# Kernel optimization log

Hardware: AMD Instinct MI355X
Metric: run time of the kernel (lower is better)

Reference implementation:

```python
import jax, jax.numpy as jnp
import numpy as np

TOP_K = 8  # num_experts_per_tok


def setup_inputs() -> dict:
    key = jax.random.key(0)
    k1, k2 = jax.random.split(key)
    hidden_states = jax.random.normal(k1, (4, 4096, 2048), dtype=jnp.float32)
    weight = jax.random.normal(k2, (128, 2048), dtype=jnp.float32) * 0.02
    return {"hidden_states": hidden_states, "weight": weight}


def reference(hidden_states, weight):
    B, S, H = hidden_states.shape
    x = hidden_states.reshape(-1, H).astype(jnp.float32)        # [T, H], T = B*S
    logits = jnp.einsum("th,eh->te", x, weight.astype(jnp.float32))  # [T, E]
    scores = jax.nn.softmax(logits, axis=-1)                    # float32 softmax
    topk_weight, topk_idx = jax.lax.top_k(scores, TOP_K)        # [T, K]
    # norm_topk_prob=True: renormalize selected probabilities
    topk_weight = topk_weight / jnp.sum(topk_weight, axis=-1, keepdims=True)
    return topk_idx, topk_weight
```

## Files before the change

### kernel.cpp

```cpp
#include <hip/hip_runtime.h>
#include <math.h>

#define T_TOKENS 16384
#define HDIM     2048
#define NEXP     128
#define TOPK     8

#define BK    64
#define NCH   (HDIM / BK)
#define KPAD  72

#define F16_MIN_NORM    6.1035156e-05f
#define SPLIT_SCALE     4096.0f
#define INV_SPLIT_SCALE 2.44140625e-04f

typedef __attribute__((ext_vector_type(8))) _Float16 f16x8;
typedef __attribute__((ext_vector_type(4))) float    f32x4;

__device__ __forceinline__ void f16split(float f, _Float16& hi, _Float16& lo) {
    _Float16 h = (_Float16)f;
    float back = (float)h;
    if (fabsf(f) < F16_MIN_NORM) { h = (_Float16)0.f; back = 0.f; }
    lo = (_Float16)((f - back) * SPLIT_SCALE);
    hi = h;
}

__global__ __launch_bounds__(256) void pack_w(const float* __restrict__ w,
                                              unsigned short* __restrict__ wp1,
                                              unsigned short* __restrict__ wp2) {
    int p = blockIdx.x * 256 + threadIdx.x;
    int lane = p & 63, nt = (p >> 6) & 7, kk = p >> 9;
    int col = lane & 15, quad = lane >> 4;
    const float* src = w + (size_t)(nt * 16 + col) * HDIM + kk * 32 + quad * 8;
    unsigned short h[8], l[8];
#pragma unroll
    for (int j = 0; j < 8; ++j) {
        _Float16 hh, ll;
        f16split(src[j], hh, ll);
        union { _Float16 x; unsigned short u; } ch, cl;
        ch.x = hh; cl.x = ll;
        h[j] = ch.u; l[j] = cl.u;
    }
    *(uint4*)(wp1 + (size_t)p * 8) = *(const uint4*)h;
    *(uint4*)(wp2 + (size_t)p * 8) = *(const uint4*)l;
}

__global__ __launch_bounds__(256, 2) void moe_gate(const float* __restrict__ x,
                                                   const unsigned short* __restrict__ wp1,
                                                   const unsigned short* __restrict__ wp2,
                                                   float* __restrict__ out_idx,
                                                   float* __restrict__ out_w) {
    __shared__ __align__(16) unsigned char smem[18432];
    unsigned short* xbuf[2][2];
    xbuf[0][0] = (unsigned short*)smem;
    xbuf[0][1] = (unsigned short*)(smem + 4608);
    xbuf[1][0] = (unsigned short*)(smem + 9216);
    xbuf[1][1] = (unsigned short*)(smem + 13824);
    float* epil = (float*)smem;

    const int tid  = threadIdx.x;
    const int lane = tid & 63;
    const int wv   = tid >> 6;
    const int col  = lane & 15;
    const int quad = lane >> 4;
    const long tok0 = (long)blockIdx.x * 32;

    const int srow = tid >> 3, scol = (tid & 7) * 8;
    const float* xg = x + (tok0 + srow) * HDIM + scol;
    const int swoff = srow * KPAD + scol;

    f32x4 acc[2][2], accc[2][2];
#pragma unroll
    for (int m = 0; m < 2; ++m)
#pragma unroll
        for (int n = 0; n < 2; ++n) { acc[m][n] = (f32x4){0,0,0,0}; accc[m][n] = (f32x4){0,0,0,0}; }

    float4 xv0, xv1;

    auto cvt_store = [&](int buf) {
        const float f[8] = {xv0.x, xv0.y, xv0.z, xv0.w, xv1.x, xv1.y, xv1.z, xv1.w};
        unsigned short h[8], l[8];
#pragma unroll
        for (int j = 0; j < 8; ++j) {
            _Float16 hh, ll;
            f16split(f[j], hh, ll);
            union { _Float16 x; unsigned short u; } ch, cl;
            ch.x = hh; cl.x = ll;
            h[j] = ch.u; l[j] = cl.u;
        }
        *(uint4*)(xbuf[buf][0] + swoff) = *(const uint4*)h;
        *(uint4*)(xbuf[buf][1] + swoff) = *(const uint4*)l;
    };

    xv0 = *(const float4*)(xg);
    xv1 = *(const float4*)(xg + 4);
    cvt_store(0);
    __syncthreads();

    for (int ch = 0; ch < NCH; ++ch) {
        const int cur = ch & 1;
        if (ch + 1 < NCH) {
            xv0 = *(const float4*)(xg + (ch + 1) * BK);
            xv1 = *(const float4*)(xg + (ch + 1) * BK + 4);
        }

        f16x8 b1[2][2], b2[2][2];
#pragma unroll
        for (int ks = 0; ks < 2; ++ks)
#pragma unroll
            for (int n = 0; n < 2; ++n) {
                const size_t off = ((size_t)((2 * ch + ks) * 8 + (wv * 2 + n)) * 64 + lane) * 8;
                b1[ks][n] = *(const f16x8*)(wp1 + off);
                b2[ks][n] = *(const f16x8*)(wp2 + off);
            }

#pragma unroll
        for (int ks = 0; ks < 2; ++ks) {
            f16x8 a1[2], a2[2];
#pragma unroll
            for (int m = 0; m < 2; ++m) {
                const int ao = (m * 16 + col) * KPAD + ks * 32 + quad * 8;
                a1[m] = *(const f16x8*)(xbuf[cur][0] + ao);
                a2[m] = *(const f16x8*)(xbuf[cur][1] + ao);
            }
#pragma unroll
            for (int m = 0; m < 2; ++m)
#pragma unroll
                for (int n = 0; n < 2; ++n) {
                    acc[m][n]  = __builtin_amdgcn_mfma_f32_16x16x32_f16(a1[m], b1[ks][n], acc[m][n],  0, 0, 0);
                    accc[m][n] = __builtin_amdgcn_mfma_f32_16x16x32_f16(a1[m], b2[ks][n], accc[m][n], 0, 0, 0);
                    accc[m][n] = __builtin_amdgcn_mfma_f32_16x16x32_f16(a2[m], b1[ks][n], accc[m][n], 0, 0, 0);
                }
        }

        if (ch + 1 < NCH) cvt_store(cur ^ 1);
        __syncthreads();
    }

#pragma unroll
    for (int m = 0; m < 2; ++m)
#pragma unroll
        for (int n = 0; n < 2; ++n)
#pragma unroll
            for (int r = 0; r < 4; ++r)
                epil[(m * 16 + quad * 4 + r) * 132 + wv * 32 + n * 16 + col] =
                    acc[m][n][r] + accc[m][n][r] * INV_SPLIT_SCALE;
    __syncthreads();

    for (int i = 0; i < 8; ++i) {
        const int t = wv * 8 + i;
        float2 p = *(const float2*)(epil + t * 132 + 2 * lane);
        float v0 = p.x, v1 = p.y;
        const int i0 = 2 * lane, i1 = 2 * lane + 1;

        float topv[TOPK];
        int topi[TOPK];
#pragma unroll
        for (int s = 0; s < TOPK; ++s) {
            float mv = (v0 >= v1) ? v0 : v1;
            int   mi = (v0 >= v1) ? i0 : i1;
#pragma unroll
            for (int off = 32; off >= 1; off >>= 1) {
                float ov = __shfl_xor(mv, off);
                int   oi = __shfl_xor(mi, off);
                if (ov > mv || (ov == mv && oi < mi)) { mv = ov; mi = oi; }
            }
            topv[s] = mv; topi[s] = mi;
            if (i0 == mi) v0 = -INFINITY;
            if (i1 == mi) v1 = -INFINITY;
        }

        const float m = topv[0];
        float sum = 0.f;
#pragma unroll
        for (int s = 0; s < TOPK; ++s) sum += expf(topv[s] - m);
        const float inv = 1.f / sum;

        float myv = topv[0]; int myi = topi[0];
#pragma unroll
        for (int s = 1; s < TOPK; ++s)
            if (lane == s) { myv = topv[s]; myi = topi[s]; }

        if (lane < TOPK) {
            long tok = tok0 + t;
            out_idx[tok * TOPK + lane] = (float)myi;
            out_w[tok * TOPK + lane]   = expf(myv - m) * inv;
        }
    }
}

extern "C" void kernel_launch(void* const* d_in, const int* in_sizes, int n_in,
                              void* d_out, int out_size, void* d_ws, size_t ws_size,
                              hipStream_t stream) {
    const float* x = (const float*)d_in[0];
    const float* w = (const float*)d_in[1];
    float* out = (float*)d_out;

    unsigned short* wp1 = (unsigned short*)d_ws;
    unsigned short* wp2 = wp1 + (size_t)NEXP * HDIM;

    pack_w<<<(64 * 8 * 64) / 256, 256, 0, stream>>>(w, wp1, wp2);
    moe_gate<<<T_TOKENS / 32, 256, 0, stream>>>(x, wp1, wp2, out, out + (size_t)T_TOKENS * TOPK);
}
```

Before: 264.8 us.

## Split K across waves per 16-token block and reduce partials in shared memory

```diff
diff --git a/kernel.cpp b/kernel.cpp
--- a/kernel.cpp
+++ b/kernel.cpp
@@ -6,9 +6,11 @@
 #define NEXP     128
 #define TOPK     8
 
-#define BK    64
-#define NCH   (HDIM / BK)
-#define KPAD  72
+#define KSPLIT   4
+#define KRANGE   (HDIM / KSPLIT)
+#define BK       64
+#define NCHW     (KRANGE / BK)
+#define KPAD     72
 
 #define F16_MIN_NORM    6.1035156e-05f
 #define SPLIT_SCALE     4096.0f
@@ -16,6 +18,7 @@
 
 typedef __attribute__((ext_vector_type(8))) _Float16 f16x8;
 typedef __attribute__((ext_vector_type(4))) float    f32x4;
+typedef __attribute__((ext_vector_type(4))) float    f32x4v;
 
 __device__ __forceinline__ void f16split(float f, _Float16& hi, _Float16& lo) {
     _Float16 h = (_Float16)f;
@@ -45,17 +48,12 @@
     *(uint4*)(wp2 + (size_t)p * 8) = *(const uint4*)l;
 }
 
-__global__ __launch_bounds__(256, 2) void moe_gate(const float* __restrict__ x,
+__global__ __launch_bounds__(256, 4) void moe_gate(const float* __restrict__ x,
                                                    const unsigned short* __restrict__ wp1,
                                                    const unsigned short* __restrict__ wp2,
                                                    float* __restrict__ out_idx,
                                                    float* __restrict__ out_w) {
-    __shared__ __align__(16) unsigned char smem[18432];
-    unsigned short* xbuf[2][2];
-    xbuf[0][0] = (unsigned short*)smem;
-    xbuf[0][1] = (unsigned short*)(smem + 4608);
-    xbuf[1][0] = (unsigned short*)(smem + 9216);
-    xbuf[1][1] = (unsigned short*)(smem + 13824);
+    __shared__ __align__(16) unsigned char smem[33792];
     float* epil = (float*)smem;
 
     const int tid  = threadIdx.x;
@@ -63,94 +61,77 @@
     const int wv   = tid >> 6;
     const int col  = lane & 15;
     const int quad = lane >> 4;
-    const long tok0 = (long)blockIdx.x * 32;
+    const long tok0 = (long)blockIdx.x * 16;
+    const int kbase = wv * KRANGE;
 
-    const int srow = tid >> 3, scol = (tid & 7) * 8;
-    const float* xg = x + (tok0 + srow) * HDIM + scol;
-    const int swoff = srow * KPAD + scol;
+    unsigned short* buf0 = (unsigned short*)(smem + wv * 4608);
+    unsigned short* buf1 = (unsigned short*)(smem + wv * 4608 + 2304);
 
-    f32x4 acc[2][2], accc[2][2];
+    const int srow = lane >> 2, scol = (lane & 3) * 16;
+    const float* xg = x + (tok0 + srow) * HDIM + kbase + scol;
+    const int woff = srow * KPAD + scol;
+
+    f32x4 acc[8], accc[8];
 #pragma unroll
-    for (int m = 0; m < 2; ++m)
+    for (int n = 0; n < 8; ++n) { acc[n] = (f32x4){0,0,0,0}; accc[n] = (f32x4){0,0,0,0}; }
+
+    for (int ch = 0; ch < NCHW; ++ch) {
+        f32x4v xv[4];
 #pragma unroll
-        for (int n = 0; n < 2; ++n) { acc[m][n] = (f32x4){0,0,0,0}; accc[m][n] = (f32x4){0,0,0,0}; }
+        for (int j = 0; j < 4; ++j)
+            xv[j] = __builtin_nontemporal_load((const f32x4v*)(xg + ch * BK + 4 * j));
 
-    float4 xv0, xv1;
-
-    auto cvt_store = [&](int buf) {
-        const float f[8] = {xv0.x, xv0.y, xv0.z, xv0.w, xv1.x, xv1.y, xv1.z, xv1.w};
-        unsigned short h[8], l[8];
+        unsigned short h[16], l[16];
 #pragma unroll
-        for (int j = 0; j < 8; ++j) {
+        for (int j = 0; j < 16; ++j) {
             _Float16 hh, ll;
-            f16split(f[j], hh, ll);
-            union { _Float16 x; unsigned short u; } ch, cl;
-            ch.x = hh; cl.x = ll;
-            h[j] = ch.u; l[j] = cl.u;
+            f16split(xv[j >> 2][j & 3], hh, ll);
+            union { _Float16 x; unsigned short u; } ch_, cl_;
+            ch_.x = hh; cl_.x = ll;
+            h[j] = ch_.u; l[j] = cl_.u;
         }
-        *(uint4*)(xbuf[buf][0] + swoff) = *(const uint4*)h;
-        *(uint4*)(xbuf[buf][1] + swoff) = *(const uint4*)l;
-    };
-
-    xv0 = *(const float4*)(xg);
-    xv1 = *(const float4*)(xg + 4);
-    cvt_store(0);
-    __syncthreads();
-
-    for (int ch = 0; ch < NCH; ++ch) {
-        const int cur = ch & 1;
-        if (ch + 1 < NCH) {
-            xv0 = *(const float4*)(xg + (ch + 1) * BK);
-            xv1 = *(const float4*)(xg + (ch + 1) * BK + 4);
-        }
-
-        f16x8 b1[2][2], b2[2][2];
-#pragma unroll
-        for (int ks = 0; ks < 2; ++ks)
-#pragma unroll
-            for (int n = 0; n < 2; ++n) {
-                const size_t off = ((size_t)((2 * ch + ks) * 8 + (wv * 2 + n)) * 64 + lane) * 8;
-                b1[ks][n] = *(const f16x8*)(wp1 + off);
-                b2[ks][n] = *(const f16x8*)(wp2 + off);
-            }
+        *(uint4*)(buf0 + woff)     = *(const uint4*)(h);
+        *(uint4*)(buf0 + woff + 8) = *(const uint4*)(h + 8);
+        *(uint4*)(buf1 + woff)     = *(const uint4*)(l);
+        *(uint4*)(buf1 + woff + 8) = *(const uint4*)(l + 8);
+        __builtin_amdgcn_wave_barrier();
 
 #pragma unroll
         for (int ks = 0; ks < 2; ++ks) {
-            f16x8 a1[2], a2[2];
+            const int kk = wv * 16 + ch * 2 + ks;
+            f16x8 a1 = *(const f16x8*)(buf0 + col * KPAD + ks * 32 + quad * 8);
+            f16x8 a2 = *(const f16x8*)(buf1 + col * KPAD + ks * 32 + quad * 8);
 #pragma unroll
-            for (int m = 0; m < 2; ++m) {
-                const int ao = (m * 16 + col) * KPAD + ks * 32 + quad * 8;
-                a1[m] = *(const f16x8*)(xbuf[cur][0] + ao);
-                a2[m] = *(const f16x8*)(xbuf[cur][1] + ao);
+            for (int nt = 0; nt < 8; ++nt) {
+                const size_t off = ((size_t)(kk * 8 + nt) * 64 + lane) * 8;
+                f16x8 b1 = *(const f16x8*)(wp1 + off);
+                f16x8 b2 = *(const f16x8*)(wp2 + off);
+                acc[nt]  = __builtin_amdgcn_mfma_f32_16x16x32_f16(a1, b1, acc[nt],  0, 0, 0);
+                accc[nt] = __builtin_amdgcn_mfma_f32_16x16x32_f16(a1, b2, accc[nt], 0, 0, 0);
+                accc[nt] = __builtin_amdgcn_mfma_f32_16x16x32_f16(a2, b1, accc[nt], 0, 0, 0);
             }
-#pragma unroll
-            for (int m = 0; m < 2; ++m)
-#pragma unroll
-                for (int n = 0; n < 2; ++n) {
-                    acc[m][n]  = __builtin_amdgcn_mfma_f32_16x16x32_f16(a1[m], b1[ks][n], acc[m][n],  0, 0, 0);
-                    accc[m][n] = __builtin_amdgcn_mfma_f32_16x16x32_f16(a1[m], b2[ks][n], accc[m][n], 0, 0, 0);
-                    accc[m][n] = __builtin_amdgcn_mfma_f32_16x16x32_f16(a2[m], b1[ks][n], accc[m][n], 0, 0, 0);
-                }
         }
-
-        if (ch + 1 < NCH) cvt_store(cur ^ 1);
-        __syncthreads();
+        __builtin_amdgcn_wave_barrier();
     }
 
-#pragma unroll
-    for (int m = 0; m < 2; ++m)
-#pragma unroll
-        for (int n = 0; n < 2; ++n)
-#pragma unroll
-            for (int r = 0; r < 4; ++r)
-                epil[(m * 16 + quad * 4 + r) * 132 + wv * 32 + n * 16 + col] =
-                    acc[m][n][r] + accc[m][n][r] * INV_SPLIT_SCALE;
     __syncthreads();
 
-    for (int i = 0; i < 8; ++i) {
-        const int t = wv * 8 + i;
-        float2 p = *(const float2*)(epil + t * 132 + 2 * lane);
-        float v0 = p.x, v1 = p.y;
+#pragma unroll
+    for (int nt = 0; nt < 8; ++nt)
+#pragma unroll
+        for (int r = 0; r < 4; ++r)
+            epil[(wv * 16 + quad * 4 + r) * 132 + nt * 16 + col] =
+                acc[nt][r] + accc[nt][r] * INV_SPLIT_SCALE;
+    __syncthreads();
+
+    for (int i = 0; i < 4; ++i) {
+        const int t = wv * 4 + i;
+        float v0 = 0.f, v1 = 0.f;
+#pragma unroll
+        for (int q = 0; q < KSPLIT; ++q) {
+            float2 p = *(const float2*)(epil + (q * 16 + t) * 132 + 2 * lane);
+            v0 += p.x; v1 += p.y;
+        }
         const int i0 = 2 * lane, i1 = 2 * lane + 1;
 
         float topv[TOPK];
@@ -200,5 +181,5 @@
     unsigned short* wp2 = wp1 + (size_t)NEXP * HDIM;
 
     pack_w<<<(64 * 8 * 64) / 256, 256, 0, stream>>>(w, wp1, wp2);
-    moe_gate<<<T_TOKENS / 32, 256, 0, stream>>>(x, wp1, wp2, out, out + (size_t)T_TOKENS * TOPK);
+    moe_gate<<<T_TOKENS / 16, 256, 0, stream>>>(x, wp1, wp2, out, out + (size_t)T_TOKENS * TOPK);
 }
```

Result: faster. 254.6 us (-3.8%).

## Stage packed weight chunks into LDS via global_load_lds and single-buffer the A tile

Applied to the files above, without the earlier changes.

```diff
diff --git a/kernel.cpp b/kernel.cpp
--- a/kernel.cpp
+++ b/kernel.cpp
@@ -8,7 +8,6 @@
 
 #define BK    64
 #define NCH   (HDIM / BK)
-#define KPAD  72
 
 #define F16_MIN_NORM    6.1035156e-05f
 #define SPLIT_SCALE     4096.0f
@@ -50,12 +49,11 @@
                                                    const unsigned short* __restrict__ wp2,
                                                    float* __restrict__ out_idx,
                                                    float* __restrict__ out_w) {
-    __shared__ __align__(16) unsigned char smem[18432];
-    unsigned short* xbuf[2][2];
-    xbuf[0][0] = (unsigned short*)smem;
-    xbuf[0][1] = (unsigned short*)(smem + 4608);
-    xbuf[1][0] = (unsigned short*)(smem + 9216);
-    xbuf[1][1] = (unsigned short*)(smem + 13824);
+    __shared__ __align__(16) unsigned char smem[40960];
+    unsigned short* a1 = (unsigned short*)smem;
+    unsigned short* a2 = (unsigned short*)(smem + 4096);
+    unsigned short* b1 = (unsigned short*)(smem + 8192);
+    unsigned short* b2 = (unsigned short*)(smem + 24576);
     float* epil = (float*)smem;
 
     const int tid  = threadIdx.x;
@@ -65,9 +63,10 @@
     const int quad = lane >> 4;
     const long tok0 = (long)blockIdx.x * 32;
 
-    const int srow = tid >> 3, scol = (tid & 7) * 8;
-    const float* xg = x + (tok0 + srow) * HDIM + scol;
-    const int swoff = srow * KPAD + scol;
+    const int srow = tid >> 3, skseg = tid & 7;
+    const float* xg = x + (tok0 + srow) * HDIM + skseg * 8;
+    const int kk_l = skseg >> 2, quad_s = skseg & 3;
+    const int adst = (((kk_l * 2 + (srow >> 4)) * 64) + quad_s * 16 + (srow & 15)) * 8;
 
     f32x4 acc[2][2], accc[2][2];
 #pragma unroll
@@ -75,65 +74,68 @@
 #pragma unroll
         for (int n = 0; n < 2; ++n) { acc[m][n] = (f32x4){0,0,0,0}; accc[m][n] = (f32x4){0,0,0,0}; }
 
-    float4 xv0, xv1;
-
-    auto cvt_store = [&](int buf) {
-        const float f[8] = {xv0.x, xv0.y, xv0.z, xv0.w, xv1.x, xv1.y, xv1.z, xv1.w};
+    f32x4 xv0, xv1;
+
+    auto load_x = [&](int ch) {
+        xv0 = *(const f32x4*)(xg + ch * BK);
+        xv1 = *(const f32x4*)(xg + ch * BK + 4);
+    };
+
+    auto cvt_store = [&]() {
         unsigned short h[8], l[8];
 #pragma unroll
         for (int j = 0; j < 8; ++j) {
             _Float16 hh, ll;
-            f16split(f[j], hh, ll);
-            union { _Float16 x; unsigned short u; } ch, cl;
-            ch.x = hh; cl.x = ll;
-            h[j] = ch.u; l[j] = cl.u;
-        }
-        *(uint4*)(xbuf[buf][0] + swoff) = *(const uint4*)h;
-        *(uint4*)(xbuf[buf][1] + swoff) = *(const uint4*)l;
+            f16split(j < 4 ? xv0[j] : xv1[j - 4], hh, ll);
+            union { _Float16 x; unsigned short u; } ch_, cl_;
+            ch_.x = hh; cl_.x = ll;
+            h[j] = ch_.u; l[j] = cl_.u;
+        }
+        *(uint4*)(a1 + adst) = *(const uint4*)h;
+        *(uint4*)(a2 + adst) = *(const uint4*)l;
     };
 
-    xv0 = *(const float4*)(xg);
-    xv1 = *(const float4*)(xg + 4);
-    cvt_store(0);
-    __syncthreads();
-
+    load_x(0);
     for (int ch = 0; ch < NCH; ++ch) {
-        const int cur = ch & 1;
-        if (ch + 1 < NCH) {
-            xv0 = *(const float4*)(xg + (ch + 1) * BK);
-            xv1 = *(const float4*)(xg + (ch + 1) * BK + 4);
-        }
-
-        f16x8 b1[2][2], b2[2][2];
-#pragma unroll
-        for (int ks = 0; ks < 2; ++ks)
+        cvt_store();
+        {
+            const unsigned short* s1 = wp1 + (size_t)ch * 8192;
+            const unsigned short* s2 = wp2 + (size_t)ch * 8192;
+#pragma unroll
+            for (int i = 0; i < 4; ++i) {
+                const int off = (i * 256 + tid) * 8;
+                __builtin_amdgcn_global_load_lds((const __attribute__((address_space(1))) void*)(s1 + off),
+                                                 (__attribute__((address_space(3))) void*)(b1 + off), 16, 0, 0);
+                __builtin_amdgcn_global_load_lds((const __attribute__((address_space(1))) void*)(s2 + off),
+                                                 (__attribute__((address_space(3))) void*)(b2 + off), 16, 0, 0);
+            }
+        }
+        __syncthreads();
+        if (ch + 1 < NCH) load_x(ch + 1);
+
+#pragma unroll
+        for (int kk = 0; kk < 2; ++kk) {
+            f16x8 af1[2], af2[2];
+#pragma unroll
+            for (int m = 0; m < 2; ++m) {
+                const int ao = ((kk * 2 + m) * 64 + lane) * 8;
+                af1[m] = *(const f16x8*)(a1 + ao);
+                af2[m] = *(const f16x8*)(a2 + ao);
+            }
 #pragma unroll
             for (int n = 0; n < 2; ++n) {
-                const size_t off = ((size_t)((2 * ch + ks) * 8 + (wv * 2 + n)) * 64 + lane) * 8;
-                b1[ks][n] = *(const f16x8*)(wp1 + off);
-                b2[ks][n] = *(const f16x8*)(wp2 + off);
-            }
-
-#pragma unroll
-        for (int ks = 0; ks < 2; ++ks) {
-            f16x8 a1[2], a2[2];
-#pragma unroll
-            for (int m = 0; m < 2; ++m) {
-                const int ao = (m * 16 + col) * KPAD + ks * 32 + quad * 8;
-                a1[m] = *(const f16x8*)(xbuf[cur][0] + ao);
-                a2[m] = *(const f16x8*)(xbuf[cur][1] + ao);
-            }
-#pragma unroll
-            for (int m = 0; m < 2; ++m)
-#pragma unroll
-                for (int n = 0; n < 2; ++n) {
-                    acc[m][n]  = __builtin_amdgcn_mfma_f32_16x16x32_f16(a1[m], b1[ks][n], acc[m][n],  0, 0, 0);
-                    accc[m][n] = __builtin_amdgcn_mfma_f32_16x16x32_f16(a1[m], b2[ks][n], accc[m][n], 0, 0, 0);
-                    accc[m][n] = __builtin_amdgcn_mfma_f32_16x16x32_f16(a2[m], b1[ks][n], accc[m][n], 0, 0, 0);
+                const int nt = 2 * wv + n;
+                const int bo = ((kk * 8 + nt) * 64 + lane) * 8;
+                f16x8 bf1 = *(const f16x8*)(b1 + bo);
+                f16x8 bf2 = *(const f16x8*)(b2 + bo);
+#pragma unroll
+                for (int m = 0; m < 2; ++m) {
+                    acc[m][n]  = __builtin_amdgcn_mfma_f32_16x16x32_f16(af1[m], bf1, acc[m][n],  0, 0, 0);
+                    accc[m][n] = __builtin_amdgcn_mfma_f32_16x16x32_f16(af1[m], bf2, accc[m][n], 0, 0, 0);
+                    accc[m][n] = __builtin_amdgcn_mfma_f32_16x16x32_f16(af2[m], bf1, accc[m][n], 0, 0, 0);
                 }
-        }
-
-        if (ch + 1 < NCH) cvt_store(cur ^ 1);
+            }
+        }
         __syncthreads();
     }
 
@@ -143,7 +145,7 @@
         for (int n = 0; n < 2; ++n)
 #pragma unroll
             for (int r = 0; r < 4; ++r)
-                epil[(m * 16 + quad * 4 + r) * 132 + wv * 32 + n * 16 + col] =
+                epil[(m * 16 + quad * 4 + r) * 132 + (2 * wv + n) * 16 + col] =
                     acc[m][n][r] + accc[m][n][r] * INV_SPLIT_SCALE;
     __syncthreads();
 
```

Measured after the change: 250.5 us. -5.4%, faster.
